# Optimization experiments

Measured on AMD Instinct MI355X. Metric: run time of the kernel, lower is better.

The kernel has to match this reference:

```python
import jax, jax.numpy as jnp
import numpy as np

N_DOMAINS = 8
LN_EPS = 1e-5


def setup_inputs() -> dict:
    key = jax.random.key(0)
    ks = jax.random.split(key, 4)
    N, D_IN, D_HID, D_OUT = 32768, 256, 1024, 256
    x = jax.random.normal(ks[0], (N, D_IN), dtype=jnp.float32)
    domain_types = jax.random.randint(ks[1], (N,), 0, N_DOMAINS, dtype=jnp.int32)
    # Per-domain MLP parameters (8 independent experts)
    W1 = jax.random.normal(ks[2], (N_DOMAINS, D_IN, D_HID), dtype=jnp.float32) * (1.0 / np.sqrt(D_IN))
    b1 = jnp.zeros((N_DOMAINS, D_HID), dtype=jnp.float32)
    gamma = jnp.ones((N_DOMAINS, D_HID), dtype=jnp.float32)
    beta = jnp.zeros((N_DOMAINS, D_HID), dtype=jnp.float32)
    W2 = jax.random.normal(ks[3], (N_DOMAINS, D_HID, D_OUT), dtype=jnp.float32) * (1.0 / np.sqrt(D_HID))
    b2 = jnp.zeros((N_DOMAINS, D_OUT), dtype=jnp.float32)
    return {"x": x, "domain_types": domain_types, "W1": W1, "b1": b1,
            "gamma": gamma, "beta": beta, "W2": W2, "b2": b2}


def _expert_mlp(x, W1d, b1d, gd, bd, W2d, b2d):
    # Linear -> LayerNorm -> ReLU -> (Dropout: identity at eval) -> Linear
    h = x @ W1d + b1d                       # [N, hid]
    mu = jnp.mean(h, axis=-1, keepdims=True)
    var = jnp.mean(jnp.square(h - mu), axis=-1, keepdims=True)
    h = (h - mu) * jax.lax.rsqrt(var + LN_EPS) * gd + bd
    h = jax.nn.relu(h)
    return h @ W2d + b2d                    # [N, out]


def reference(x, domain_types, W1, b1, gamma, beta, W2, b2):
    # output dim == x.shape[-1] (as in the torch code: zeros(batch, x.shape[-1]))
    out = jnp.zeros((x.shape[0], x.shape[-1]), dtype=x.dtype)
    for d in range(N_DOMAINS):  # small fixed expert loop (static MoE dispatch)
        y = _expert_mlp(x, W1[d], b1[d], gamma[d], beta[d], W2[d], b2[d])
        mask = (domain_types == d)[:, None]
        out = jnp.where(mask, y, out)
    return out
```

## Files before the change

### kernel.cpp

```cpp
#include <hip/hip_runtime.h>
#include <hip/hip_bf16.h>


#define ND 8
#define NROWS 32768
#define DIN 256
#define DHID 1024
#define DOUT 256
#define MPAD 33792
#define NTILES 264

typedef short short8 __attribute__((ext_vector_type(8)));
typedef float floatx4 __attribute__((ext_vector_type(4)));

__device__ __forceinline__ unsigned short f2bf(float f) {
    unsigned u = __builtin_bit_cast(unsigned, f);
    unsigned r = u + 0x7fff + ((u >> 16) & 1);
    return (unsigned short)(r >> 16);
}
__device__ __forceinline__ float bf2f(unsigned short h) {
    unsigned u = ((unsigned)h) << 16;
    return __builtin_bit_cast(float, u);
}

#define GLDS16(gp, lp) __builtin_amdgcn_global_load_lds( \
    (const __attribute__((address_space(1))) void*)(gp), \
    (__attribute__((address_space(3))) void*)(lp), 16, 0, 0)

__global__ void transpose_bf16(const float* __restrict__ in,
                               unsigned short* __restrict__ out,
                               int R, int C) {
    __shared__ float t[32][33];
    const int z = blockIdx.z;
    const int c0 = blockIdx.x * 32, r0 = blockIdx.y * 32;
    const int tx = threadIdx.x & 31, ty = threadIdx.x >> 5;
    const float* src = in + (size_t)z * R * C;
    unsigned short* dst = out + (size_t)z * R * C;
#pragma unroll
    for (int i = 0; i < 32; i += 8)
        t[ty + i][tx] = src[(size_t)(r0 + ty + i) * C + c0 + tx];
    __syncthreads();
#pragma unroll
    for (int i = 0; i < 32; i += 8)
        dst[(size_t)(c0 + ty + i) * R + r0 + tx] = f2bf(t[tx][ty + i]);
}

__global__ void zero_init(int* __restrict__ perm, int* __restrict__ cnt) {
    int i = blockIdx.x * 256 + threadIdx.x;
    if (i < MPAD) perm[i] = -1;
    if (i < 16) cnt[i] = 0;
}

__global__ void histo(const int* __restrict__ dt, int* __restrict__ counts) {
    __shared__ int lc[ND];
    if (threadIdx.x < ND) lc[threadIdx.x] = 0;
    __syncthreads();
    int i = blockIdx.x * 256 + threadIdx.x;
    atomicAdd(&lc[dt[i]], 1);
    __syncthreads();
    if (threadIdx.x < ND) atomicAdd(&counts[threadIdx.x], lc[threadIdx.x]);
}

__global__ void make_meta(const int* __restrict__ counts, int* __restrict__ cursors,
                          int2* __restrict__ meta) {
    if (threadIdx.x == 0 && blockIdx.x == 0) {
        int off = 0, t = 0;
        for (int d = 0; d < ND; d++) {
            cursors[d] = off;
            int nt = (counts[d] + 127) >> 7;
            for (int i = 0; i < nt; i++) meta[t++] = make_int2(d, off + (i << 7));
            off += nt << 7;
        }
        for (; t < NTILES; t++) meta[t] = make_int2(-1, 0);
    }
}

__global__ __launch_bounds__(256)
void assign_pos(const int* __restrict__ dt, int* __restrict__ cursors,
                int* __restrict__ perm, int* __restrict__ pos) {
    __shared__ int lcnt[ND];
    __shared__ int lbase[ND];
    const int tid = threadIdx.x;
    if (tid < ND) lcnt[tid] = 0;
    __syncthreads();
    const int r = blockIdx.x * 256 + tid;
    const int d = dt[r];
    const int myrank = atomicAdd(&lcnt[d], 1);
    __syncthreads();
    if (tid < ND && lcnt[tid] > 0)
        lbase[tid] = atomicAdd(&cursors[tid], lcnt[tid]);
    __syncthreads();
    const int p = lbase[d] + myrank;
    pos[r] = p;
    perm[p] = r;
}

__global__ __launch_bounds__(256)
void copy_rows(const float* __restrict__ x, const int* __restrict__ pos,
               unsigned short* __restrict__ xs) {
    const int tid = threadIdx.x;
    const int lane = tid & 63;
    const int r = blockIdx.x * 4 + (tid >> 6);
    const int p = pos[r];
    float4 v = ((const float4*)(x + (size_t)r * DIN))[lane];
    ushort4 o;
    o.x = f2bf(v.x); o.y = f2bf(v.y); o.z = f2bf(v.z); o.w = f2bf(v.w);
    ((ushort4*)(xs + (size_t)p * DIN))[lane] = o;
}

template <int K, bool ISB>
__global__ __launch_bounds__(256, 2)
void gemm_bt(const unsigned short* __restrict__ A,
             const unsigned short* __restrict__ Bt,
             const float* __restrict__ bias,
             const int2* __restrict__ meta,
             const int* __restrict__ perm,
             unsigned short* __restrict__ Cbf,
             float* __restrict__ Cf,
             const int Ntot,
             float2* __restrict__ spart,
             const float* __restrict__ gamma,
             const float* __restrict__ beta) {
    const int2 md = meta[blockIdx.x];
    const int dom = md.x;
    if (dom < 0) return;
    const int m0 = md.y;
    const int n0 = blockIdx.y * 128;

    __shared__ unsigned short As[128 * 32];
    __shared__ unsigned short Bs[128 * 32];
    __shared__ float sred[2][128];

    const int tid = threadIdx.x;
    const int lane = tid & 63;
    const int w = tid >> 6;
    const int wr = w >> 1, wc = w & 1;

    const unsigned short* Abase = A + (size_t)m0 * K;
    const unsigned short* Bbase = Bt + (size_t)dom * Ntot * K + (size_t)n0 * K;

    if (!ISB) {
        if (tid < 128) { sred[0][tid] = 0.f; sred[1][tid] = 0.f; }
    }

    const int ma = (w * 128 + lane) >> 2;
    const int kc = lane & 3;
    float muv[2], rsv[2];
    if (ISB) {
#pragma unroll
        for (int h2 = 0; h2 < 2; ++h2) {
            const int rm = m0 + ma + h2 * 16;
            float s = 0.f, s2 = 0.f;
#pragma unroll
            for (int nb = 0; nb < 8; ++nb) {
                const float2 p = spart[(size_t)nb * MPAD + rm];
                s += p.x; s2 += p.y;
            }
            const float mu = s * (1.f / 1024.f);
            const float var = fmaxf(s2 * (1.f / 1024.f) - mu * mu, 0.f);
            muv[h2] = mu;
            rsv[h2] = rsqrtf(var + 1e-5f);
        }
    }

    floatx4 acc[4][4];
#pragma unroll
    for (int i = 0; i < 4; i++)
#pragma unroll
        for (int j = 0; j < 4; j++) acc[i][j] = 0.f;

    for (int k0 = 0; k0 < K; k0 += 32) {
        if (!ISB) {
#pragma unroll
            for (int it = 0; it < 2; ++it) {
                const int c = w * 128 + it * 64 + lane;
                const int m = c >> 2, kcc = c & 3;
                GLDS16(Abase + (size_t)m * K + k0 + kcc * 8, &As[(w * 128 + it * 64) * 8]);
            }
        } else {
            const float* gp = gamma + dom * DHID + k0 + kc * 8;
            const float* bp = beta + dom * DHID + k0 + kc * 8;
            const float4 g0 = ((const float4*)gp)[0];
            const float4 g1 = ((const float4*)gp)[1];
            const float4 e0 = ((const float4*)bp)[0];
            const float4 e1 = ((const float4*)bp)[1];
#pragma unroll
            for (int h2 = 0; h2 < 2; ++h2) {
                const int m = ma + h2 * 16;
                const short8 hv = *(const short8*)(Abase + (size_t)m * K + k0 + kc * 8);
                const float mu = muv[h2], rs = rsv[h2];
                short8 o;
                o[0] = (short)f2bf(fmaxf((bf2f((unsigned short)hv[0]) - mu) * rs * g0.x + e0.x, 0.f));
                o[1] = (short)f2bf(fmaxf((bf2f((unsigned short)hv[1]) - mu) * rs * g0.y + e0.y, 0.f));
                o[2] = (short)f2bf(fmaxf((bf2f((unsigned short)hv[2]) - mu) * rs * g0.z + e0.z, 0.f));
                o[3] = (short)f2bf(fmaxf((bf2f((unsigned short)hv[3]) - mu) * rs * g0.w + e0.w, 0.f));
                o[4] = (short)f2bf(fmaxf((bf2f((unsigned short)hv[4]) - mu) * rs * g1.x + e1.x, 0.f));
                o[5] = (short)f2bf(fmaxf((bf2f((unsigned short)hv[5]) - mu) * rs * g1.y + e1.y, 0.f));
                o[6] = (short)f2bf(fmaxf((bf2f((unsigned short)hv[6]) - mu) * rs * g1.z + e1.z, 0.f));
                o[7] = (short)f2bf(fmaxf((bf2f((unsigned short)hv[7]) - mu) * rs * g1.w + e1.w, 0.f));
                *(short8*)&As[(w * 128 + h2 * 64 + lane) * 8] = o;
            }
        }
#pragma unroll
        for (int it = 0; it < 2; ++it) {
            const int c = w * 128 + it * 64 + lane;
            const int m = c >> 2, kcc = c & 3;
            GLDS16(Bbase + (size_t)m * K + k0 + kcc * 8, &Bs[(w * 128 + it * 64) * 8]);
        }
        __syncthreads();

        short8 a[4], b[4];
        const int kk = (lane >> 4) * 8;
#pragma unroll
        for (int i = 0; i < 4; i++) {
            const int m = wr * 64 + i * 16 + (lane & 15);
            a[i] = *(const short8*)&As[m * 32 + kk];
            const int n = wc * 64 + i * 16 + (lane & 15);
            b[i] = *(const short8*)&Bs[n * 32 + kk];
        }
#pragma unroll
        for (int i = 0; i < 4; i++)
#pragma unroll
            for (int j = 0; j < 4; j++)
                acc[i][j] = __builtin_amdgcn_mfma_f32_16x16x32_bf16(a[i], b[j], acc[i][j], 0, 0, 0);
        __syncthreads();
    }

    const int quad = lane >> 4;
    const int l15 = lane & 15;
    if (!ISB) {
        float bv[4];
#pragma unroll
        for (int j = 0; j < 4; j++)
            bv[j] = bias[dom * Ntot + n0 + wc * 64 + j * 16 + l15];
#pragma unroll
        for (int i = 0; i < 4; i++) {
#pragma unroll
            for (int r = 0; r < 4; r++) {
                const int rl = wr * 64 + i * 16 + quad * 4 + r;
                float s = 0.f, s2 = 0.f;
#pragma unroll
                for (int j = 0; j < 4; j++) {
                    const float v = acc[i][j][r] + bv[j];
                    Cbf[(size_t)(m0 + rl) * Ntot + n0 + wc * 64 + j * 16 + l15] = f2bf(v);
                    s += v; s2 += v * v;
                }
#pragma unroll
                for (int o = 8; o; o >>= 1) {
                    s  += __shfl_xor(s, o, 64);
                    s2 += __shfl_xor(s2, o, 64);
                }
                if (l15 == 0) {
                    atomicAdd(&sred[0][rl], s);
                    atomicAdd(&sred[1][rl], s2);
                }
            }
        }
        __syncthreads();
        if (tid < 128)
            spart[(size_t)blockIdx.y * MPAD + m0 + tid] =
                make_float2(sred[0][tid], sred[1][tid]);
    } else {
#pragma unroll
        for (int i = 0; i < 4; i++) {
            const int rowbase = m0 + wr * 64 + i * 16 + quad * 4;
#pragma unroll
            for (int r = 0; r < 4; r++) {
                const int orig = perm[rowbase + r];
                if (orig < 0) continue;
#pragma unroll
                for (int j = 0; j < 4; j++) {
                    const int col = n0 + wc * 64 + j * 16 + l15;
                    Cf[(size_t)orig * Ntot + col] = acc[i][j][r] + bias[dom * Ntot + col];
                }
            }
        }
    }
}

extern "C" void kernel_launch(void* const* d_in, const int* in_sizes, int n_in,
                              void* d_out, int out_size, void* d_ws, size_t ws_size,
                              hipStream_t stream) {
    const float* x = (const float*)d_in[0];
    const int* dt = (const int*)d_in[1];
    const float* W1 = (const float*)d_in[2];
    const float* b1 = (const float*)d_in[3];
    const float* gamma = (const float*)d_in[4];
    const float* beta = (const float*)d_in[5];
    const float* W2 = (const float*)d_in[6];
    const float* b2 = (const float*)d_in[7];
    float* out = (float*)d_out;

    char* ws = (char*)d_ws;
    size_t off = 0;
    auto take = [&](size_t nbytes) -> char* {
        char* p = ws + off;
        off = (off + nbytes + 255) & ~(size_t)255;
        return p;
    };
    unsigned short* W1T = (unsigned short*)take((size_t)ND * DHID * DIN * 2);
    unsigned short* W2T = (unsigned short*)take((size_t)ND * DOUT * DHID * 2);
    unsigned short* XS  = (unsigned short*)take((size_t)MPAD * DIN * 2);
    unsigned short* H   = (unsigned short*)take((size_t)MPAD * DHID * 2);
    float2* SPART = (float2*)take((size_t)8 * MPAD * 8);
    int* PERM   = (int*)take(MPAD * 4);
    int* POS    = (int*)take(NROWS * 4);
    int* CNT    = (int*)take(64);
    int2* META  = (int2*)take(NTILES * 8);
    (void)ws_size; (void)n_in; (void)in_sizes; (void)out_size;

    int* COUNTS = CNT;
    int* CURSORS = CNT + 8;

    transpose_bf16<<<dim3(DHID / 32, DIN / 32, ND), 256, 0, stream>>>(W1, W1T, DIN, DHID);
    transpose_bf16<<<dim3(DOUT / 32, DHID / 32, ND), 256, 0, stream>>>(W2, W2T, DHID, DOUT);
    zero_init<<<(MPAD + 255) / 256, 256, 0, stream>>>(PERM, CNT);
    histo<<<NROWS / 256, 256, 0, stream>>>(dt, COUNTS);
    make_meta<<<1, 1, 0, stream>>>(COUNTS, CURSORS, META);
    assign_pos<<<NROWS / 256, 256, 0, stream>>>(dt, CURSORS, PERM, POS);
    copy_rows<<<NROWS / 4, 256, 0, stream>>>(x, POS, XS);
    gemm_bt<DIN, false><<<dim3(NTILES, DHID / 128), 256, 0, stream>>>(
        XS, W1T, b1, META, nullptr, H, nullptr, DHID, SPART, nullptr, nullptr);
    gemm_bt<DHID, true><<<dim3(NTILES, DOUT / 128), 256, 0, stream>>>(
        H, W2T, b2, META, PERM, nullptr, out, DOUT, SPART, gamma, beta);
}
```

Measured before the change: 221.8 us.

## Merge setup kernels and prefetch next LayerNorm tile in second GEMM

Folds the two weight transposes into a single launch, merges zero-init with the histogram, and parallelises the tile-metadata builder across 64 threads, cutting launch count and serial work. In the second GEMM, the hidden activations and gamma/beta for the next k-step are loaded into registers before the MFMA loop body (software prefetch). The B-tile async loads are also issued before the normalisation, so they overlap with it. This raises register pressure, and zeroing the counters inside the transpose kernel relies on stream ordering ahead of the histogram.

Measured after the change: 212.9 us. 1.04x faster.

```diff
diff --git a/kernel.cpp b/kernel.cpp
--- a/kernel.cpp
+++ b/kernel.cpp
@@ -27,12 +27,22 @@
     (const __attribute__((address_space(1))) void*)(gp), \
     (__attribute__((address_space(3))) void*)(lp), 16, 0, 0)
 
-__global__ void transpose_bf16(const float* __restrict__ in,
-                               unsigned short* __restrict__ out,
-                               int R, int C) {
+__global__ void transpose_both(const float* __restrict__ W1, unsigned short* __restrict__ W1T,
+                               const float* __restrict__ W2, unsigned short* __restrict__ W2T,
+                               int* __restrict__ cnt) {
+    if (blockIdx.x == 0 && threadIdx.x < 16) cnt[threadIdx.x] = 0;
     __shared__ float t[32][33];
-    const int z = blockIdx.z;
-    const int c0 = blockIdx.x * 32, r0 = blockIdx.y * 32;
+    int b = blockIdx.x;
+    const float* in; unsigned short* out; int R, C, bx, by, z;
+    if (b < 2048) {
+        in = W1; out = W1T; R = DIN; C = DHID;
+        bx = b & 31; by = (b >> 5) & 7; z = b >> 8;
+    } else {
+        b -= 2048;
+        in = W2; out = W2T; R = DHID; C = DOUT;
+        bx = b & 7; by = (b >> 3) & 31; z = b >> 8;
+    }
+    const int c0 = bx * 32, r0 = by * 32;
     const int tx = threadIdx.x & 31, ty = threadIdx.x >> 5;
     const float* src = in + (size_t)z * R * C;
     unsigned short* dst = out + (size_t)z * R * C;
@@ -45,33 +55,41 @@
         dst[(size_t)(c0 + ty + i) * R + r0 + tx] = f2bf(t[tx][ty + i]);
 }
 
-__global__ void zero_init(int* __restrict__ perm, int* __restrict__ cnt) {
-    int i = blockIdx.x * 256 + threadIdx.x;
+__global__ void init_histo(const int* __restrict__ dt, int* __restrict__ perm,
+                           int* __restrict__ counts) {
+    const int i = blockIdx.x * 256 + threadIdx.x;
     if (i < MPAD) perm[i] = -1;
-    if (i < 16) cnt[i] = 0;
-}
-
-__global__ void histo(const int* __restrict__ dt, int* __restrict__ counts) {
     __shared__ int lc[ND];
     if (threadIdx.x < ND) lc[threadIdx.x] = 0;
     __syncthreads();
-    int i = blockIdx.x * 256 + threadIdx.x;
-    atomicAdd(&lc[dt[i]], 1);
-    __syncthreads();
-    if (threadIdx.x < ND) atomicAdd(&counts[threadIdx.x], lc[threadIdx.x]);
+    if (i < NROWS) atomicAdd(&lc[dt[i]], 1);
+    __syncthreads();
+    if (threadIdx.x < ND && lc[threadIdx.x] > 0)
+        atomicAdd(&counts[threadIdx.x], lc[threadIdx.x]);
 }
 
 __global__ void make_meta(const int* __restrict__ counts, int* __restrict__ cursors,
                           int2* __restrict__ meta) {
-    if (threadIdx.x == 0 && blockIdx.x == 0) {
-        int off = 0, t = 0;
+    __shared__ int base[ND], ntc[ND];
+    const int t = threadIdx.x;
+    if (t == 0) {
+        int off = 0;
         for (int d = 0; d < ND; d++) {
+            base[d] = off;
+            ntc[d] = (counts[d] + 127) >> 7;
             cursors[d] = off;
-            int nt = (counts[d] + 127) >> 7;
-            for (int i = 0; i < nt; i++) meta[t++] = make_int2(d, off + (i << 7));
-            off += nt << 7;
-        }
-        for (; t < NTILES; t++) meta[t] = make_int2(-1, 0);
+            off += ntc[d] << 7;
+        }
+    }
+    __syncthreads();
+    for (int i = t; i < NTILES; i += 64) {
+        int2 m = make_int2(-1, 0);
+#pragma unroll
+        for (int d = 0; d < ND; d++) {
+            const int ti = i - (base[d] >> 7);
+            if (ti >= 0 && ti < ntc[d]) m = make_int2(d, base[d] + (ti << 7));
+        }
+        meta[i] = m;
     }
 }
 
@@ -146,6 +164,8 @@
     const int ma = (w * 128 + lane) >> 2;
     const int kc = lane & 3;
     float muv[2], rsv[2];
+    short8 hv0{}, hv1{};
+    float4 gc0{}, gc1{}, ec0{}, ec1{};
     if (ISB) {
 #pragma unroll
         for (int h2 = 0; h2 < 2; ++h2) {
@@ -161,6 +181,12 @@
             muv[h2] = mu;
             rsv[h2] = rsqrtf(var + 1e-5f);
         }
+        const float* gp = gamma + dom * DHID + kc * 8;
+        const float* bp = beta + dom * DHID + kc * 8;
+        gc0 = ((const float4*)gp)[0]; gc1 = ((const float4*)gp)[1];
+        ec0 = ((const float4*)bp)[0]; ec1 = ((const float4*)bp)[1];
+        hv0 = *(const short8*)(Abase + (size_t)ma * K + kc * 8);
+        hv1 = *(const short8*)(Abase + (size_t)(ma + 16) * K + kc * 8);
     }
 
     floatx4 acc[4][4];
@@ -170,6 +196,12 @@
         for (int j = 0; j < 4; j++) acc[i][j] = 0.f;
 
     for (int k0 = 0; k0 < K; k0 += 32) {
+#pragma unroll
+        for (int it = 0; it < 2; ++it) {
+            const int c = w * 128 + it * 64 + lane;
+            const int m = c >> 2, kcc = c & 3;
+            GLDS16(Bbase + (size_t)m * K + k0 + kcc * 8, &Bs[(w * 128 + it * 64) * 8]);
+        }
         if (!ISB) {
 #pragma unroll
             for (int it = 0; it < 2; ++it) {
@@ -178,36 +210,36 @@
                 GLDS16(Abase + (size_t)m * K + k0 + kcc * 8, &As[(w * 128 + it * 64) * 8]);
             }
         } else {
-            const float* gp = gamma + dom * DHID + k0 + kc * 8;
-            const float* bp = beta + dom * DHID + k0 + kc * 8;
-            const float4 g0 = ((const float4*)gp)[0];
-            const float4 g1 = ((const float4*)gp)[1];
-            const float4 e0 = ((const float4*)bp)[0];
-            const float4 e1 = ((const float4*)bp)[1];
+            const float gA[8] = {gc0.x, gc0.y, gc0.z, gc0.w, gc1.x, gc1.y, gc1.z, gc1.w};
+            const float eA[8] = {ec0.x, ec0.y, ec0.z, ec0.w, ec1.x, ec1.y, ec1.z, ec1.w};
 #pragma unroll
             for (int h2 = 0; h2 < 2; ++h2) {
-                const int m = ma + h2 * 16;
-                const short8 hv = *(const short8*)(Abase + (size_t)m * K + k0 + kc * 8);
                 const float mu = muv[h2], rs = rsv[h2];
+                const short8 hvv = h2 ? hv1 : hv0;
                 short8 o;
-                o[0] = (short)f2bf(fmaxf((bf2f((unsigned short)hv[0]) - mu) * rs * g0.x + e0.x, 0.f));
-                o[1] = (short)f2bf(fmaxf((bf2f((unsigned short)hv[1]) - mu) * rs * g0.y + e0.y, 0.f));
-                o[2] = (short)f2bf(fmaxf((bf2f((unsigned short)hv[2]) - mu) * rs * g0.z + e0.z, 0.f));
-                o[3] = (short)f2bf(fmaxf((bf2f((unsigned short)hv[3]) - mu) * rs * g0.w + e0.w, 0.f));
-                o[4] = (short)f2bf(fmaxf((bf2f((unsigned short)hv[4]) - mu) * rs * g1.x + e1.x, 0.f));
-                o[5] = (short)f2bf(fmaxf((bf2f((unsigned short)hv[5]) - mu) * rs * g1.y + e1.y, 0.f));
-                o[6] = (short)f2bf(fmaxf((bf2f((unsigned short)hv[6]) - mu) * rs * g1.z + e1.z, 0.f));
-                o[7] = (short)f2bf(fmaxf((bf2f((unsigned short)hv[7]) - mu) * rs * g1.w + e1.w, 0.f));
+#pragma unroll
+                for (int e = 0; e < 8; ++e) {
+                    const float rg = gA[e] * rs;
+                    const float v = fmaxf(fmaf(bf2f((unsigned short)hvv[e]), rg,
+                                               fmaf(-mu, rg, eA[e])), 0.f);
+                    o[e] = (short)f2bf(v);
+                }
                 *(short8*)&As[(w * 128 + h2 * 64 + lane) * 8] = o;
             }
         }
-#pragma unroll
-        for (int it = 0; it < 2; ++it) {
-            const int c = w * 128 + it * 64 + lane;
-            const int m = c >> 2, kcc = c & 3;
-            GLDS16(Bbase + (size_t)m * K + k0 + kcc * 8, &Bs[(w * 128 + it * 64) * 8]);
-        }
         __syncthreads();
+
+        short8 nh0{}, nh1{};
+        float4 ng0{}, ng1{}, ne0{}, ne1{};
+        const bool more = ISB && (k0 + 32 < K);
+        if (more) {
+            const float* gp = gamma + dom * DHID + k0 + 32 + kc * 8;
+            const float* bp = beta + dom * DHID + k0 + 32 + kc * 8;
+            ng0 = ((const float4*)gp)[0]; ng1 = ((const float4*)gp)[1];
+            ne0 = ((const float4*)bp)[0]; ne1 = ((const float4*)bp)[1];
+            nh0 = *(const short8*)(Abase + (size_t)ma * K + k0 + 32 + kc * 8);
+            nh1 = *(const short8*)(Abase + (size_t)(ma + 16) * K + k0 + 32 + kc * 8);
+        }
 
         short8 a[4], b[4];
         const int kk = (lane >> 4) * 8;
@@ -224,6 +256,8 @@
             for (int j = 0; j < 4; j++)
                 acc[i][j] = __builtin_amdgcn_mfma_f32_16x16x32_bf16(a[i], b[j], acc[i][j], 0, 0, 0);
         __syncthreads();
+
+        if (more) { hv0 = nh0; hv1 = nh1; gc0 = ng0; gc1 = ng1; ec0 = ne0; ec1 = ne1; }
     }
 
     const int quad = lane >> 4;
@@ -312,11 +346,9 @@
     int* COUNTS = CNT;
     int* CURSORS = CNT + 8;
 
-    transpose_bf16<<<dim3(DHID / 32, DIN / 32, ND), 256, 0, stream>>>(W1, W1T, DIN, DHID);
-    transpose_bf16<<<dim3(DOUT / 32, DHID / 32, ND), 256, 0, stream>>>(W2, W2T, DHID, DOUT);
-    zero_init<<<(MPAD + 255) / 256, 256, 0, stream>>>(PERM, CNT);
-    histo<<<NROWS / 256, 256, 0, stream>>>(dt, COUNTS);
-    make_meta<<<1, 1, 0, stream>>>(COUNTS, CURSORS, META);
+    transpose_both<<<4096, 256, 0, stream>>>(W1, W1T, W2, W2T, CNT);
+    init_histo<<<MPAD / 256, 256, 0, stream>>>(dt, PERM, COUNTS);
+    make_meta<<<1, 64, 0, stream>>>(COUNTS, CURSORS, META);
     assign_pos<<<NROWS / 256, 256, 0, stream>>>(dt, CURSORS, PERM, POS);
     copy_rows<<<NROWS / 4, 256, 0, stream>>>(x, POS, XS);
     gemm_bt<DIN, false><<<dim3(NTILES, DHID / 128), 256, 0, stream>>>(
```
